# Performance work log

Hardware: AMD Instinct MI355X
Metric: run time of the kernel (lower is better)

The kernel has to match this reference:

```python
import jax, jax.numpy as jnp
import numpy as np

B, P, D, H, U, C = 32, 196, 512, 8, 4, 500

def setup_inputs() -> dict:
    key = jax.random.key(0)
    ks = jax.random.split(key, 12)
    s = 0.02
    return {
        "patch_embeddings": jax.random.normal(ks[0], (B, P, D), jnp.float32),
        "global_features": jax.random.normal(ks[1], (B, D), jnp.float32),
        "query_vectors": jax.random.normal(ks[2], (H, D), jnp.float32) * s,
        "dom_W": jax.random.normal(ks[3], (D, D), jnp.float32) / np.sqrt(D),
        "dom_b": jnp.zeros((D,), jnp.float32),
        "sem_W": jax.random.normal(ks[4], (H, D, D), jnp.float32) / np.sqrt(D),
        "sem_b": jnp.zeros((H, D), jnp.float32),
        "unknown_semantic_tokens": jax.random.normal(ks[5], (U, D), jnp.float32) * s,
        "known_prefix": jax.random.normal(ks[6], (C, 1, D), jnp.float32) * s,   # SOS embedding per class
        "known_suffix": jax.random.normal(ks[7], (C, 1, D), jnp.float32) * s,   # last-token embedding per class
        "unk_prefix": jax.random.normal(ks[8], (1, D), jnp.float32) * s,
        "unk_suffix": jax.random.normal(ks[9], (1, D), jnp.float32) * s,
    }


def reference(patch_embeddings, global_features, query_vectors, dom_W, dom_b,
              sem_W, sem_b, unknown_semantic_tokens, known_prefix, known_suffix,
              unk_prefix, unk_suffix):
    b, p, d = patch_embeddings.shape
    h = query_vectors.shape[0]
    c = known_prefix.shape[0]
    u = unknown_semantic_tokens.shape[0]

    # SemanticTokenExtractor: per-head attention over patches (vectorized over heads)
    scores = jnp.einsum('bpd,hd->bph', patch_embeddings, query_vectors)      # [B,P,H]
    weights = jax.nn.softmax(scores, axis=1)                                  # softmax over patches
    semantic_tokens = jnp.einsum('bph,bpd->bhd', weights, patch_embeddings)   # [B,H,D]

    # DomainTokenGenerator (2D input -> identity) + domain projection (torch Linear: x @ W.T + b)
    projected_domain = global_features @ dom_W.T + dom_b                      # [B,D]

    # Per-head semantic projections: head k uses its own Linear
    projected_sem = jnp.einsum('bhd,hed->bhe', semantic_tokens, sem_W) + sem_b  # [B,H,D]

    # Known prompts: for each (b, c): [prefix_c(1), domain_b(1), semantics_b(H), suffix_c(1)]
    pre = jnp.broadcast_to(known_prefix[None], (b, c, 1, d))
    dom = jnp.broadcast_to(projected_domain[:, None, None, :], (b, c, 1, d))
    sem = jnp.broadcast_to(projected_sem[:, None], (b, c, h, d))
    suf = jnp.broadcast_to(known_suffix[None], (b, c, 1, d))
    known_prompts = jnp.concatenate([pre, dom, sem, suf], axis=2).reshape(b * c, h + 3, d)

    # Unknown prompts: [unk_prefix(1), domain_b(1), unknown_semantic_tokens(U), unk_suffix(1)]
    upre = jnp.broadcast_to(unk_prefix[None], (b, 1, d))
    udom = projected_domain[:, None, :]
    usem = jnp.broadcast_to(unknown_semantic_tokens[None], (b, u, d))
    usuf = jnp.broadcast_to(unk_suffix[None], (b, 1, d))
    unknown_prompts = jnp.concatenate([upre, udom, usem, usuf], axis=1)       # [B, U+3, D]

    return known_prompts, unknown_prompts, semantic_tokens
```

## Files before the change

### kernel.cpp

```cpp
#include <hip/hip_runtime.h>

typedef unsigned int uint32;
typedef uint32 v4u __attribute__((ext_vector_type(4)));

#define Bb 32
#define Pp 196
#define Dd 512
#define Hh 8
#define Uu 4
#define Cc 500

#define OUT1_ELEM_OFF 90112000
#define OUT2_ELEM_OFF 90226688

#define NPC 16

#define WS_SC   0
#define WS_PART 51200
#define WS_DOM  2148352
#define WS_SEM  2164736

__device__ __forceinline__ float dot4(float4 a, float4 b, float acc) {
    acc = fmaf(a.x, b.x, acc);
    acc = fmaf(a.y, b.y, acc);
    acc = fmaf(a.z, b.z, acc);
    acc = fmaf(a.w, b.w, acc);
    return acc;
}

__global__ __launch_bounds__(256)
void k_scores(const float* __restrict__ patch, const float* __restrict__ query,
              float* __restrict__ sc) {
    __shared__ float s_q[Hh * Dd];
    const int b = blockIdx.x / 49;
    const int p0 = (blockIdx.x % 49) * 4;
    const int tid = threadIdx.x;
    for (int j = tid; j < Hh * Dd / 4; j += 256)
        ((float4*)s_q)[j] = ((const float4*)query)[j];
    __syncthreads();

    const int wave = tid >> 6, lane = tid & 63;
    const int p = p0 + wave;
    const float* pr = patch + ((size_t)b * Pp + p) * Dd + lane * 8;
    const float4 v0 = *(const float4*)pr;
    const float4 v1 = *(const float4*)(pr + 4);

    float out = 0.f;
#pragma unroll
    for (int h = 0; h < 8; ++h) {
        const float4 q0 = *(const float4*)&s_q[h * Dd + lane * 8];
        const float4 q1 = *(const float4*)&s_q[h * Dd + lane * 8 + 4];
        float a = dot4(v0, q0, 0.f);
        a = dot4(v1, q1, a);
#pragma unroll
        for (int m = 32; m >= 1; m >>= 1) a += __shfl_xor(a, m, 64);
        if (lane == h) out = a;
    }
    if (lane < 8) sc[((size_t)b * Hh + lane) * Pp + p] = out;
}

__global__ __launch_bounds__(256)
void k_pool_part(const float* __restrict__ patch, const float* __restrict__ sc,
                 float* __restrict__ part) {
    __shared__ float s_w[Hh * Pp];
    const int b = blockIdx.x >> 4;
    const int pc = blockIdx.x & 15;
    const int tid = threadIdx.x;

    for (int j = tid; j < Hh * Pp; j += 256) s_w[j] = sc[(size_t)b * Hh * Pp + j];
    __syncthreads();

    {
        const int h = tid >> 5, gl = tid & 31;
        float m = -1e30f;
        for (int p = gl; p < Pp; p += 32) m = fmaxf(m, s_w[h * Pp + p]);
#pragma unroll
        for (int mm = 16; mm >= 1; mm >>= 1) m = fmaxf(m, __shfl_xor(m, mm, 64));
        float s = 0.f;
        for (int p = gl; p < Pp; p += 32) s += __expf(s_w[h * Pp + p] - m);
#pragma unroll
        for (int mm = 16; mm >= 1; mm >>= 1) s += __shfl_xor(s, mm, 64);
        const float inv = 1.f / s;
        for (int p = gl; p < Pp; p += 32)
            s_w[h * Pp + p] = __expf(s_w[h * Pp + p] - m) * inv;
    }
    __syncthreads();

    const int f = tid & 127;
    const int hq = tid >> 7;
    const int pstart = pc * 13;
    const int pend = (pstart + 13 < Pp) ? pstart + 13 : Pp;
    float4 a0 = {0, 0, 0, 0}, a1 = a0, a2 = a0, a3 = a0;
    const float4* pb4 = (const float4*)(patch + (size_t)b * Pp * Dd);
    for (int p = pstart; p < pend; ++p) {
        const float4 pv = pb4[p * 128 + f];
        const float w0 = s_w[(hq * 4 + 0) * Pp + p];
        const float w1 = s_w[(hq * 4 + 1) * Pp + p];
        const float w2 = s_w[(hq * 4 + 2) * Pp + p];
        const float w3 = s_w[(hq * 4 + 3) * Pp + p];
        a0.x = fmaf(w0, pv.x, a0.x); a0.y = fmaf(w0, pv.y, a0.y);
        a0.z = fmaf(w0, pv.z, a0.z); a0.w = fmaf(w0, pv.w, a0.w);
        a1.x = fmaf(w1, pv.x, a1.x); a1.y = fmaf(w1, pv.y, a1.y);
        a1.z = fmaf(w1, pv.z, a1.z); a1.w = fmaf(w1, pv.w, a1.w);
        a2.x = fmaf(w2, pv.x, a2.x); a2.y = fmaf(w2, pv.y, a2.y);
        a2.z = fmaf(w2, pv.z, a2.z); a2.w = fmaf(w2, pv.w, a2.w);
        a3.x = fmaf(w3, pv.x, a3.x); a3.y = fmaf(w3, pv.y, a3.y);
        a3.z = fmaf(w3, pv.z, a3.z); a3.w = fmaf(w3, pv.w, a3.w);
    }
    float4* po = (float4*)part + ((size_t)b * NPC + pc) * 1024;
    po[(hq * 4 + 0) * 128 + f] = a0;
    po[(hq * 4 + 1) * 128 + f] = a1;
    po[(hq * 4 + 2) * 128 + f] = a2;
    po[(hq * 4 + 3) * 128 + f] = a3;
}

__global__ __launch_bounds__(256)
void k_combine(const float* __restrict__ part, float* __restrict__ st) {
    const int idx = blockIdx.x * 256 + threadIdx.x;
    const int b = idx >> 10;
    const int r = idx & 1023;
    const float4* p4 = (const float4*)part;
    float4 a = {0, 0, 0, 0};
#pragma unroll
    for (int pc = 0; pc < NPC; ++pc) {
        const float4 v = p4[((size_t)b * NPC + pc) * 1024 + r];
        a.x += v.x; a.y += v.y; a.z += v.z; a.w += v.w;
    }
    ((float4*)st)[idx] = a;
}

#define PJS 516
__global__ __launch_bounds__(256)
void k_proj(const float* __restrict__ gf, const float* __restrict__ domW,
            const float* __restrict__ domb, const float* __restrict__ semW,
            const float* __restrict__ semb, const float* __restrict__ st,
            float* __restrict__ dom_ws, float* __restrict__ sem_ws) {
    __shared__ float s_w[32 * PJS];
    __shared__ float s_st[32 * PJS];
    const int blk = blockIdx.x;
    const int tid = threadIdx.x;
    if (blk < 128) {
        const int h = blk >> 4;
        const int e0 = (blk & 15) * 32;
        for (int g = tid; g < 32 * 128; g += 256) {
            const int r = g >> 7, c4 = g & 127;
            const float4 w = ((const float4*)semW)[((size_t)(h * Dd + e0 + r)) * 128 + c4];
            *(float4*)&s_w[r * PJS + c4 * 4] = w;
            const float4 s = ((const float4*)st)[((size_t)(r * Hh + h)) * 128 + c4];
            *(float4*)&s_st[r * PJS + c4 * 4] = s;
        }
        __syncthreads();
        const int pe = tid & 15;
        const int pb = tid >> 4;
        const float* w0r = &s_w[pe * PJS];
        const float* w1r = &s_w[(pe + 16) * PJS];
        const float* s0r = &s_st[pb * PJS];
        const float* s1r = &s_st[(pb + 16) * PJS];
        float a00 = 0.f, a01 = 0.f, a10 = 0.f, a11 = 0.f;
#pragma unroll 4
        for (int d = 0; d < Dd; d += 4) {
            const float4 w0 = *(const float4*)&w0r[d];
            const float4 w1 = *(const float4*)&w1r[d];
            const float4 s0 = *(const float4*)&s0r[d];
            const float4 s1 = *(const float4*)&s1r[d];
            a00 = dot4(s0, w0, a00);
            a01 = dot4(s0, w1, a01);
            a10 = dot4(s1, w0, a10);
            a11 = dot4(s1, w1, a11);
        }
        const int e_ = e0 + pe;
        const float b0 = semb[h * Dd + e_], b1 = semb[h * Dd + e_ + 16];
        sem_ws[((size_t)pb * Hh + h) * Dd + e_]             = a00 + b0;
        sem_ws[((size_t)pb * Hh + h) * Dd + e_ + 16]        = a01 + b1;
        sem_ws[((size_t)(pb + 16) * Hh + h) * Dd + e_]      = a10 + b0;
        sem_ws[((size_t)(pb + 16) * Hh + h) * Dd + e_ + 16] = a11 + b1;
    } else {
        const int tg = (blk - 128) * 256 + tid;
        const int b = tg >> 9;
        const int e = tg & 511;
        const float4* wr = (const float4*)(domW + (size_t)e * Dd);
        const float4* gr = (const float4*)(gf + (size_t)b * Dd);
        float acc = domb[e];
#pragma unroll 8
        for (int j = 0; j < Dd / 4; ++j) acc = dot4(gr[j], wr[j], acc);
        dom_ws[b * Dd + e] = acc;
    }
}

#define KN_CB 10
__global__ __launch_bounds__(256)
void k_assemble(const v4u* __restrict__ pre, const v4u* __restrict__ suf,
                const v4u* __restrict__ dom, const v4u* __restrict__ sem,
                const v4u* __restrict__ upre, const v4u* __restrict__ usuf,
                const v4u* __restrict__ ust,
                v4u* __restrict__ out0, v4u* __restrict__ out1) {
    __shared__ v4u s_tok[1152];
    const int blk = blockIdx.x;
    const int tid = threadIdx.x;
    if (blk < Bb * (Cc / KN_CB)) {
        const int b = blk / (Cc / KN_CB);
        const int c0 = (blk % (Cc / KN_CB)) * KN_CB;
        for (int j = tid; j < 1152; j += 256)
            s_tok[j] = (j < 128) ? dom[b * 128 + j] : sem[b * 1024 + (j - 128)];
        __syncthreads();
#pragma unroll
        for (int cj = 0; cj < KN_CB; ++cj) {
            const int c = c0 + cj;
            v4u* row = out0 + (size_t)(b * Cc + c) * 1408;
#pragma unroll
            for (int k = 0; k < 6; ++k) {
                const int i = tid + k * 256;
                if (k < 5 || i < 1408) {
                    const int t = i >> 7;
                    const int off = i & 127;
                    v4u v;
                    if (t == 0) v = pre[c * 128 + off];
                    else if (t == 10) v = suf[c * 128 + off];
                    else v = s_tok[(t - 1) * 128 + off];
                    __builtin_nontemporal_store(v, &row[i]);
                }
            }
        }
    } else {
        const int b = blk - Bb * (Cc / KN_CB);
#pragma unroll
        for (int k = 0; k < 4; ++k) {
            const int i = tid + k * 256;
            if (k < 3 || i < 896) {
                const int t = i >> 7;
                const int off = i & 127;
                v4u v;
                if (t == 0) v = upre[off];
                else if (t == 6) v = usuf[off];
                else if (t == 1) v = dom[b * 128 + off];
                else v = ust[(t - 2) * 128 + off];
                __builtin_nontemporal_store(v, &out1[b * 896 + i]);
            }
        }
    }
}

extern "C" void kernel_launch(void* const* d_in, const int* in_sizes, int n_in,
                              void* d_out, int out_size, void* d_ws, size_t ws_size,
                              hipStream_t stream) {
    const float* patch = (const float*)d_in[0];
    const float* gf    = (const float*)d_in[1];
    const float* query = (const float*)d_in[2];
    const float* domW  = (const float*)d_in[3];
    const float* domb  = (const float*)d_in[4];
    const float* semW  = (const float*)d_in[5];
    const float* semb  = (const float*)d_in[6];
    const float* ust   = (const float*)d_in[7];
    const float* pre   = (const float*)d_in[8];
    const float* suf   = (const float*)d_in[9];
    const float* upre  = (const float*)d_in[10];
    const float* usuf  = (const float*)d_in[11];

    float* out = (float*)d_out;
    float* st_out = out + OUT2_ELEM_OFF;

    float* ws   = (float*)d_ws;
    float* sc_w = ws + WS_SC;
    float* part = ws + WS_PART;
    float* domp = ws + WS_DOM;
    float* semp = ws + WS_SEM;

    hipLaunchKernelGGL(k_scores, dim3(Bb * 49), dim3(256), 0, stream, patch, query, sc_w);
    hipLaunchKernelGGL(k_pool_part, dim3(Bb * NPC), dim3(256), 0, stream, patch, sc_w, part);
    hipLaunchKernelGGL(k_combine, dim3(128), dim3(256), 0, stream, part, st_out);
    hipLaunchKernelGGL(k_proj, dim3(192), dim3(256), 0, stream,
                       gf, domW, domb, semW, semb, st_out, domp, semp);
    hipLaunchKernelGGL(k_assemble, dim3(Bb * (Cc / KN_CB) + Bb), dim3(256), 0, stream,
                       (const v4u*)pre, (const v4u*)suf,
                       (const v4u*)domp, (const v4u*)semp,
                       (const v4u*)upre, (const v4u*)usuf, (const v4u*)ust,
                       (v4u*)out, (v4u*)(out + OUT1_ELEM_OFF));
}
```

Before: 438.2 us.

## Merge pooling partials into one kernel and flatten prompt assembly into grid-stride copy

The pooling stage now computes the full weighted sum per (batch, head, feature slice) in one kernel, removing the partial-sum buffer and the separate combine kernel. Prompt assembly becomes a flat grid-stride loop over all output vectors with per-element index decoding and ordinary stores, replacing the shared-memory staged, nontemporal-store scheme. This drops one launch and workspace traffic. In exchange pooling runs on far fewer blocks (128), and assembly pays integer divisions per element and loses nontemporal stores on the roughly 360 MB write.

After: 434.3 us. About the same (-0.9%).

```diff
diff --git a/kernel.cpp b/kernel.cpp
--- a/kernel.cpp
+++ b/kernel.cpp
@@ -13,12 +13,13 @@
 #define OUT1_ELEM_OFF 90112000
 #define OUT2_ELEM_OFF 90226688
 
-#define NPC 16
+#define OUT0_V4 22528000u
+#define OUT1_V4 28672u
+#define TOT_V4  (OUT0_V4 + OUT1_V4)
 
 #define WS_SC   0
-#define WS_PART 51200
-#define WS_DOM  2148352
-#define WS_SEM  2164736
+#define WS_DOM  51200
+#define WS_SEM  67584
 
 __device__ __forceinline__ float dot4(float4 a, float4 b, float acc) {
     acc = fmaf(a.x, b.x, acc);
@@ -60,11 +61,11 @@
 }
 
 __global__ __launch_bounds__(256)
-void k_pool_part(const float* __restrict__ patch, const float* __restrict__ sc,
-                 float* __restrict__ part) {
+void k_pool(const float* __restrict__ patch, const float* __restrict__ sc,
+            float* __restrict__ st) {
     __shared__ float s_w[Hh * Pp];
-    const int b = blockIdx.x >> 4;
-    const int pc = blockIdx.x & 15;
+    const int b = blockIdx.x >> 2;
+    const int dc = blockIdx.x & 3;
     const int tid = threadIdx.x;
 
     for (int j = tid; j < Hh * Pp; j += 256) s_w[j] = sc[(size_t)b * Hh * Pp + j];
@@ -86,47 +87,20 @@
     }
     __syncthreads();
 
-    const int f = tid & 127;
-    const int hq = tid >> 7;
-    const int pstart = pc * 13;
-    const int pend = (pstart + 13 < Pp) ? pstart + 13 : Pp;
-    float4 a0 = {0, 0, 0, 0}, a1 = a0, a2 = a0, a3 = a0;
+    const int h = tid >> 5;
+    const int f = (tid & 31) + dc * 32;
     const float4* pb4 = (const float4*)(patch + (size_t)b * Pp * Dd);
-    for (int p = pstart; p < pend; ++p) {
+    float4 a = {0, 0, 0, 0};
+#pragma unroll 4
+    for (int p = 0; p < Pp; ++p) {
+        const float w = s_w[h * Pp + p];
         const float4 pv = pb4[p * 128 + f];
-        const float w0 = s_w[(hq * 4 + 0) * Pp + p];
-        const float w1 = s_w[(hq * 4 + 1) * Pp + p];
-        const float w2 = s_w[(hq * 4 + 2) * Pp + p];
-        const float w3 = s_w[(hq * 4 + 3) * Pp + p];
-        a0.x = fmaf(w0, pv.x, a0.x); a0.y = fmaf(w0, pv.y, a0.y);
-        a0.z = fmaf(w0, pv.z, a0.z); a0.w = fmaf(w0, pv.w, a0.w);
-        a1.x = fmaf(w1, pv.x, a1.x); a1.y = fmaf(w1, pv.y, a1.y);
-        a1.z = fmaf(w1, pv.z, a1.z); a1.w = fmaf(w1, pv.w, a1.w);
-        a2.x = fmaf(w2, pv.x, a2.x); a2.y = fmaf(w2, pv.y, a2.y);
-        a2.z = fmaf(w2, pv.z, a2.z); a2.w = fmaf(w2, pv.w, a2.w);
-        a3.x = fmaf(w3, pv.x, a3.x); a3.y = fmaf(w3, pv.y, a3.y);
-        a3.z = fmaf(w3, pv.z, a3.z); a3.w = fmaf(w3, pv.w, a3.w);
-    }
-    float4* po = (float4*)part + ((size_t)b * NPC + pc) * 1024;
-    po[(hq * 4 + 0) * 128 + f] = a0;
-    po[(hq * 4 + 1) * 128 + f] = a1;
-    po[(hq * 4 + 2) * 128 + f] = a2;
-    po[(hq * 4 + 3) * 128 + f] = a3;
-}
-
-__global__ __launch_bounds__(256)
-void k_combine(const float* __restrict__ part, float* __restrict__ st) {
-    const int idx = blockIdx.x * 256 + threadIdx.x;
-    const int b = idx >> 10;
-    const int r = idx & 1023;
-    const float4* p4 = (const float4*)part;
-    float4 a = {0, 0, 0, 0};
-#pragma unroll
-    for (int pc = 0; pc < NPC; ++pc) {
-        const float4 v = p4[((size_t)b * NPC + pc) * 1024 + r];
-        a.x += v.x; a.y += v.y; a.z += v.z; a.w += v.w;
-    }
-    ((float4*)st)[idx] = a;
+        a.x = fmaf(w, pv.x, a.x);
+        a.y = fmaf(w, pv.y, a.y);
+        a.z = fmaf(w, pv.z, a.z);
+        a.w = fmaf(w, pv.w, a.w);
+    }
+    ((float4*)st)[(size_t)b * 1024 + h * 128 + f] = a;
 }
 
 #define PJS 516
@@ -187,56 +161,38 @@
     }
 }
 
-#define KN_CB 10
 __global__ __launch_bounds__(256)
 void k_assemble(const v4u* __restrict__ pre, const v4u* __restrict__ suf,
                 const v4u* __restrict__ dom, const v4u* __restrict__ sem,
                 const v4u* __restrict__ upre, const v4u* __restrict__ usuf,
                 const v4u* __restrict__ ust,
-                v4u* __restrict__ out0, v4u* __restrict__ out1) {
-    __shared__ v4u s_tok[1152];
-    const int blk = blockIdx.x;
-    const int tid = threadIdx.x;
-    if (blk < Bb * (Cc / KN_CB)) {
-        const int b = blk / (Cc / KN_CB);
-        const int c0 = (blk % (Cc / KN_CB)) * KN_CB;
-        for (int j = tid; j < 1152; j += 256)
-            s_tok[j] = (j < 128) ? dom[b * 128 + j] : sem[b * 1024 + (j - 128)];
-        __syncthreads();
-#pragma unroll
-        for (int cj = 0; cj < KN_CB; ++cj) {
-            const int c = c0 + cj;
-            v4u* row = out0 + (size_t)(b * Cc + c) * 1408;
-#pragma unroll
-            for (int k = 0; k < 6; ++k) {
-                const int i = tid + k * 256;
-                if (k < 5 || i < 1408) {
-                    const int t = i >> 7;
-                    const int off = i & 127;
-                    v4u v;
-                    if (t == 0) v = pre[c * 128 + off];
-                    else if (t == 10) v = suf[c * 128 + off];
-                    else v = s_tok[(t - 1) * 128 + off];
-                    __builtin_nontemporal_store(v, &row[i]);
-                }
-            }
+                v4u* __restrict__ outv) {
+    const uint32 stride = gridDim.x * 256u;
+    for (uint32 i = blockIdx.x * 256u + threadIdx.x; i < TOT_V4; i += stride) {
+        v4u v;
+        if (i < OUT0_V4) {
+            const uint32 row = i / 1408u;
+            const uint32 rem = i - row * 1408u;
+            const uint32 t = rem >> 7;
+            const uint32 off = rem & 127u;
+            const uint32 b = row / 500u;
+            const uint32 c = row - b * 500u;
+            if (t == 0u)       v = pre[c * 128u + off];
+            else if (t == 10u) v = suf[c * 128u + off];
+            else if (t == 1u)  v = dom[b * 128u + off];
+            else               v = sem[b * 1024u + (t - 2u) * 128u + off];
+        } else {
+            const uint32 j = i - OUT0_V4;
+            const uint32 b = j / 896u;
+            const uint32 rem = j - b * 896u;
+            const uint32 t = rem >> 7;
+            const uint32 off = rem & 127u;
+            if (t == 0u)      v = upre[off];
+            else if (t == 6u) v = usuf[off];
+            else if (t == 1u) v = dom[b * 128u + off];
+            else              v = ust[(t - 2u) * 128u + off];
         }
-    } else {
-        const int b = blk - Bb * (Cc / KN_CB);
-#pragma unroll
-        for (int k = 0; k < 4; ++k) {
-            const int i = tid + k * 256;
-            if (k < 3 || i < 896) {
-                const int t = i >> 7;
-                const int off = i & 127;
-                v4u v;
-                if (t == 0) v = upre[off];
-                else if (t == 6) v = usuf[off];
-                else if (t == 1) v = dom[b * 128 + off];
-                else v = ust[(t - 2) * 128 + off];
-                __builtin_nontemporal_store(v, &out1[b * 896 + i]);
-            }
-        }
+        outv[i] = v;
     }
 }
 
@@ -261,18 +217,16 @@
 
     float* ws   = (float*)d_ws;
     float* sc_w = ws + WS_SC;
-    float* part = ws + WS_PART;
     float* domp = ws + WS_DOM;
     float* semp = ws + WS_SEM;
 
     hipLaunchKernelGGL(k_scores, dim3(Bb * 49), dim3(256), 0, stream, patch, query, sc_w);
-    hipLaunchKernelGGL(k_pool_part, dim3(Bb * NPC), dim3(256), 0, stream, patch, sc_w, part);
-    hipLaunchKernelGGL(k_combine, dim3(128), dim3(256), 0, stream, part, st_out);
+    hipLaunchKernelGGL(k_pool, dim3(Bb * 4), dim3(256), 0, stream, patch, sc_w, st_out);
     hipLaunchKernelGGL(k_proj, dim3(192), dim3(256), 0, stream,
                        gf, domW, domb, semW, semb, st_out, domp, semp);
-    hipLaunchKernelGGL(k_assemble, dim3(Bb * (Cc / KN_CB) + Bb), dim3(256), 0, stream,
+    hipLaunchKernelGGL(k_assemble, dim3(2048), dim3(256), 0, stream,
                        (const v4u*)pre, (const v4u*)suf,
                        (const v4u*)domp, (const v4u*)semp,
                        (const v4u*)upre, (const v4u*)usuf, (const v4u*)ust,
-                       (v4u*)out, (v4u*)(out + OUT1_ELEM_OFF));
-}
+                       (v4u*)out);
+}
```
